# Kernel tuning notes

Hardware: AMD Instinct MI355X
Metric: run time of the kernel (lower is better)

## Reference

```python
import jax, jax.numpy as jnp
import numpy as np

N_NODES = 50000
N_EDGES = 1600000
IN_DIM = 128
N_HEADS = 8
OUT_DIM = 16  # output_dim // n_heads = 128 // 8


def setup_inputs() -> dict:
    key = jax.random.key(0)
    ks = jax.random.split(key, 8)
    feature = jax.random.normal(ks[0], (N_NODES, IN_DIM), dtype=jnp.float32)
    edge_src = jax.random.randint(ks[1], (N_EDGES,), 0, N_NODES)
    edge_dst = jax.random.randint(ks[2], (N_EDGES,), 0, N_NODES)
    edge_weight = jax.random.uniform(ks[3], (N_EDGES,), dtype=jnp.float32)
    w_lin = jax.random.normal(ks[4], (IN_DIM, N_HEADS * OUT_DIM), dtype=jnp.float32) * 0.1
    att_l = jax.random.normal(ks[5], (N_HEADS, OUT_DIM), dtype=jnp.float32) * 0.1
    att_r = jax.random.normal(ks[6], (N_HEADS, OUT_DIM), dtype=jnp.float32) * 0.1
    w_res = jax.random.normal(ks[7], (IN_DIM, N_HEADS * OUT_DIM), dtype=jnp.float32) * 0.1
    return {"feature": feature, "edge_src": edge_src, "edge_dst": edge_dst,
            "edge_weight": edge_weight, "w_lin": w_lin, "att_l": att_l,
            "att_r": att_r, "w_res": w_res}


def reference(feature, edge_src, edge_dst, edge_weight, w_lin, att_l, att_r, w_res):
    N = feature.shape[0]
    H, C = att_l.shape
    # Linear projection -> [N, H, C]
    x = (feature @ w_lin).reshape(N, H, C)
    # Per-node attention logits [N, H]
    al = jnp.einsum('nhc,hc->nh', x, att_l)
    ar = jnp.einsum('nhc,hc->nh', x, att_r)
    # Per-edge logits: gather src/dst, weight, leaky-relu  [E, H]
    alpha = al[edge_src] + ar[edge_dst]
    alpha = edge_weight[:, None] * alpha
    alpha = jax.nn.leaky_relu(alpha, negative_slope=0.2)
    # Segment softmax over edges grouped by destination node
    m = jax.ops.segment_max(alpha, edge_dst, num_segments=N)  # [N, H]
    m = jnp.where(jnp.isfinite(m), m, 0.0)
    e = jnp.exp(alpha - m[edge_dst])
    denom = jax.ops.segment_sum(e, edge_dst, num_segments=N)  # [N, H]
    coef = e / denom[edge_dst]                                 # [E, H]
    # Message passing: gather src feats, weight by coef, scatter-sum to dst
    msg = x[edge_src] * coef[:, :, None]                       # [E, H, C]
    feat = jax.ops.segment_sum(msg, edge_dst, num_segments=N)  # [N, H, C]
    out = jax.nn.elu(feat).reshape(N, H * C)
    out = out + feature @ w_res  # residual branch
    return out
```

## Files before the change

kernel.cpp:

```cpp
#include <hip/hip_runtime.h>
#include <math.h>

#define IN_DIM 128
#define NH 8
#define OC 16
#define HC 128
#define BSTR 136
#define ECH 4096
#define BINSZ 128
#define NBINS_MAX 512
#define FSTR 132
#define ALS 32

typedef __attribute__((ext_vector_type(8))) short short8;
typedef __attribute__((ext_vector_type(4))) float f32x4;

__device__ __forceinline__ unsigned short bf16_rne(float f) {
  unsigned int u = __builtin_bit_cast(unsigned int, f);
  u += 0x7FFFu + ((u >> 16) & 1u);
  return (unsigned short)(u >> 16);
}
__device__ __forceinline__ float bf16_to_f(unsigned short h) {
  unsigned int u = ((unsigned int)h) << 16;
  return __builtin_bit_cast(float, u);
}

__global__ __launch_bounds__(256) void k1_fused(const float* __restrict__ feature,
                                                const float* __restrict__ w_lin,
                                                const float* __restrict__ w_res,
                                                const float* __restrict__ att_l,
                                                const float* __restrict__ att_r,
                                                unsigned char* __restrict__ x8,
                                                unsigned char* __restrict__ als,
                                                float* __restrict__ ar,
                                                float* __restrict__ out,
                                                int* __restrict__ bin_cursor, int N) {
  __shared__ unsigned short BL[HC * BSTR];
  __shared__ unsigned short BR[HC * BSTR];
  __shared__ unsigned short WH[16 * BSTR];
  __shared__ unsigned short WL[16 * BSTR];
  const int t = threadIdx.x;
  if (blockIdx.x == 0) {
    bin_cursor[t] = 0;
    bin_cursor[t + 256] = 0;
  }
  for (int i = t; i < IN_DIM * HC; i += 256) {
    const int r = i >> 7, c = i & 127;
    BL[c * BSTR + r] = bf16_rne(w_lin[i]);
    BR[c * BSTR + r] = bf16_rne(w_res[i]);
  }
#pragma unroll
  for (int j = 0; j < 8; ++j) {
    const int idx = t * 8 + j;
    const int k = idx >> 4, c = idx & 15;
    const int h8 = c & 7;
    const float* __restrict__ av = ((c < 8) ? att_l : att_r) + h8 * OC;
    const float* __restrict__ wr = w_lin + k * HC + h8 * OC;
    float acc = 0.f;
#pragma unroll
    for (int oc = 0; oc < 16; ++oc) acc = fmaf(wr[oc], av[oc], acc);
    const unsigned short hi = bf16_rne(acc);
    WH[c * BSTR + k] = hi;
    WL[c * BSTR + k] = bf16_rne(acc - bf16_to_f(hi));
  }
  __syncthreads();

  const int wave = t >> 6, lane = t & 63;
  const int n16 = lane & 15, quad = lane >> 4;
  const int nStrips = (N + 15) >> 4;

  for (int strip = blockIdx.x * 4 + wave; strip < nStrips; strip += gridDim.x * 4) {
    const int row0 = strip * 16;
    const int arow = row0 + n16;
    const float* __restrict__ ap =
        feature + (size_t)((arow < N) ? arow : 0) * IN_DIM + quad * 8;
    short8 ahi[4], alo[4];
#pragma unroll
    for (int ks = 0; ks < 4; ++ks) {
      const float4 f0 = *(const float4*)(ap + ks * 32);
      const float4 f1 = *(const float4*)(ap + ks * 32 + 4);
      const float fv[8] = {f0.x, f0.y, f0.z, f0.w, f1.x, f1.y, f1.z, f1.w};
      short8 h, l;
#pragma unroll
      for (int j = 0; j < 8; ++j) {
        const unsigned short hh = bf16_rne(fv[j]);
        h[j] = (short)hh;
        l[j] = (short)bf16_rne(fv[j] - bf16_to_f(hh));
      }
      ahi[ks] = h;
      alo[ks] = l;
    }
    f32x4 xacc[8];
#pragma unroll
    for (int u = 0; u < 8; ++u) xacc[u] = (f32x4){0.f, 0.f, 0.f, 0.f};
#pragma unroll
    for (int ks = 0; ks < 4; ++ks) {
#pragma unroll
      for (int u = 0; u < 8; ++u) {
        const int boff = (u * 16 + n16) * BSTR + ks * 32 + quad * 8;
        const short8 bh = *(const short8*)&BL[boff];
        xacc[u] = __builtin_amdgcn_mfma_f32_16x16x32_bf16(ahi[ks], bh, xacc[u], 0, 0, 0);
        xacc[u] = __builtin_amdgcn_mfma_f32_16x16x32_bf16(alo[ks], bh, xacc[u], 0, 0, 0);
      }
    }
    {
      f32x4 accA = {0.f, 0.f, 0.f, 0.f};
#pragma unroll
      for (int ks = 0; ks < 4; ++ks) {
        const int boff = n16 * BSTR + ks * 32 + quad * 8;
        const short8 wh = *(const short8*)&WH[boff];
        const short8 wl = *(const short8*)&WL[boff];
        accA = __builtin_amdgcn_mfma_f32_16x16x32_bf16(ahi[ks], wh, accA, 0, 0, 0);
        accA = __builtin_amdgcn_mfma_f32_16x16x32_bf16(alo[ks], wh, accA, 0, 0, 0);
        accA = __builtin_amdgcn_mfma_f32_16x16x32_bf16(ahi[ks], wl, accA, 0, 0, 0);
      }
#pragma unroll
      for (int r = 0; r < 4; ++r) {
        const int rr = row0 + quad * 4 + r;
        if (rr < N) {
          if (n16 < 8) {
            *(unsigned short*)(als + (size_t)rr * ALS + n16 * 2) = bf16_rne(accA[r]);
          } else {
            ar[(size_t)rr * NH + (n16 - 8)] = accA[r];
          }
        }
      }
    }
    float m[4];
#pragma unroll
    for (int r = 0; r < 4; ++r) {
      float mm = 0.f;
#pragma unroll
      for (int u = 0; u < 8; ++u) mm = fmaxf(mm, fabsf(xacc[u][r]));
      mm = fmaxf(mm, __shfl_xor(mm, 1));
      mm = fmaxf(mm, __shfl_xor(mm, 2));
      mm = fmaxf(mm, __shfl_xor(mm, 4));
      mm = fmaxf(mm, __shfl_xor(mm, 8));
      m[r] = mm;
    }
#pragma unroll
    for (int r = 0; r < 4; ++r) {
      const int rr = row0 + quad * 4 + r;
      if (rr < N) {
        const float inv = (m[r] > 0.f) ? 127.f / m[r] : 0.f;
#pragma unroll
        for (int u = 0; u < 8; ++u) {
          const int q8 = (int)rintf(xacc[u][r] * inv) + 128;
          x8[(size_t)rr * HC + u * 16 + n16] = (unsigned char)q8;
        }
        if (n16 == 0)
          *(float*)(als + (size_t)rr * ALS + 16) = (m[r] > 0.f) ? m[r] / 127.f : 0.f;
      }
    }
#pragma unroll
    for (int cg = 0; cg < 2; ++cg) {
      f32x4 acc[4] = {{0.f,0.f,0.f,0.f},{0.f,0.f,0.f,0.f},{0.f,0.f,0.f,0.f},{0.f,0.f,0.f,0.f}};
#pragma unroll
      for (int ks = 0; ks < 4; ++ks) {
#pragma unroll
        for (int j = 0; j < 4; ++j) {
          const int boff = ((cg * 4 + j) * 16 + n16) * BSTR + ks * 32 + quad * 8;
          const short8 bh = *(const short8*)&BR[boff];
          acc[j] = __builtin_amdgcn_mfma_f32_16x16x32_bf16(ahi[ks], bh, acc[j], 0, 0, 0);
          acc[j] = __builtin_amdgcn_mfma_f32_16x16x32_bf16(alo[ks], bh, acc[j], 0, 0, 0);
        }
      }
#pragma unroll
      for (int j = 0; j < 4; ++j) {
        const int colo = (cg * 4 + j) * 16 + n16;
#pragma unroll
        for (int r = 0; r < 4; ++r) {
          const int rr = row0 + quad * 4 + r;
          if (rr < N) out[(size_t)rr * HC + colo] = acc[j][r];
        }
      }
    }
  }
}

__global__ __launch_bounds__(1024) void kb1_scatter(const int* __restrict__ esrc,
                                                    const int* __restrict__ edst,
                                                    const float* __restrict__ ew,
                                                    int* __restrict__ bin_cursor,
                                                    uint2* __restrict__ tmp,
                                                    int E, int nbins, int cap) {
  __shared__ int cnt[NBINS_MAX];
  __shared__ int gbase[NBINS_MAX];
  const int t = threadIdx.x;
  if (t < NBINS_MAX) cnt[t] = 0;
  __syncthreads();
  const int base = blockIdx.x * ECH;
  uint2 v[4];
  int bj[4], sj[4];
#pragma unroll
  for (int j = 0; j < 4; ++j) {
    const int e = base + j * 1024 + t;
    bj[j] = -1;
    if (e < E) {
      const int d = edst[e];
      v[j] = make_uint2((unsigned)esrc[e] | ((unsigned)(d & (BINSZ - 1)) << 16),
                        __float_as_uint(ew[e]));
      bj[j] = d >> 7;
      sj[j] = atomicAdd(&cnt[bj[j]], 1);
    }
  }
  __syncthreads();
  for (int b = t; b < nbins; b += 1024) {
    const int own = cnt[b];
    if (own > 0) gbase[b] = atomicAdd(&bin_cursor[b], own);
  }
  __syncthreads();
#pragma unroll
  for (int j = 0; j < 4; ++j)
    if (bj[j] >= 0) {
      const int p = gbase[bj[j]] + sj[j];
      if (p >= 0 && p < cap) tmp[(size_t)bj[j] * cap + p] = v[j];
    }
}

__global__ __launch_bounds__(1024) void kb3_sort(const uint2* __restrict__ tmp,
                                                 const int* __restrict__ bin_cursor,
                                                 uint2* __restrict__ packed,
                                                 int* __restrict__ row_start,
                                                 int cap, int nbins, int N) {
  const int b = blockIdx.x, t = threadIdx.x;
  const int M = bin_cursor[b];
  __shared__ int redw[16];
  int part = 0;
  for (int i = t; i < b; i += 1024) part += bin_cursor[i];
#pragma unroll
  for (int o = 32; o >= 1; o >>= 1) part += __shfl_xor(part, o);
  if ((t & 63) == 0) redw[t >> 6] = part;
  __syncthreads();
  int gstart = 0;
#pragma unroll
  for (int w = 0; w < 16; ++w) gstart += redw[w];
  if (b == nbins - 1 && t == 0) row_start[N] = gstart + M;

  const uint2* __restrict__ src = tmp + (size_t)b * cap;
  __shared__ int cnt[BINSZ];
  __shared__ int cur[BINSZ];
  __shared__ int s[BINSZ];
  if (t < BINSZ) cnt[t] = 0;
  __syncthreads();
  for (int i = t; i < M; i += 1024) atomicAdd(&cnt[src[i].x >> 16], 1);
  __syncthreads();
  if (t < BINSZ) s[t] = cnt[t];
  __syncthreads();
  for (int o = 1; o < BINSZ; o <<= 1) {
    int a = 0;
    if (t < BINSZ && t >= o) a = s[t - o];
    __syncthreads();
    if (t < BINSZ) s[t] += a;
    __syncthreads();
  }
  if (t < BINSZ) {
    const int ex = s[t] - cnt[t];
    cur[t] = gstart + ex;
    const int node = b * BINSZ + t;
    if (node < N) row_start[node] = gstart + ex;
  }
  __syncthreads();
  for (int i = t; i < M; i += 1024) {
    const uint2 v = src[i];
    const int pos = atomicAdd(&cur[v.x >> 16], 1);
    packed[pos] = make_uint2(v.x & 0xFFFFu, v.y);
  }
}

__global__ __launch_bounds__(64) void k5_agg(const unsigned char* __restrict__ x8,
                                             const unsigned char* __restrict__ als,
                                             const uint2* __restrict__ packed,
                                             const int* __restrict__ row_start,
                                             const float* __restrict__ ar,
                                             float* __restrict__ out, int N) {
  const int n = blockIdx.x;
  const int l = threadIdx.x;
  const int s0 = row_start[n];
  const int En = row_start[n + 1] - s0;
  if (En == 0) return;
  __shared__ int sbuf[64];
  __shared__ float wbuf[64];
  __shared__ float scbuf[64];
  __shared__ float fred[8 * FSTR];
  const int h = l & 7;
  const int g = l >> 3;
  const int ch0 = h * 16;

  const float arn = ar[(size_t)n * NH + h];
  float dpart = 0.f;
  float facsum = 0.f;
  float f[16];
#pragma unroll
  for (int j = 0; j < 16; ++j) f[j] = 0.f;

  for (int base = 0; base < En; base += 64) {
    const int cnt = min(64, En - base);
    __syncthreads();
    if (l < cnt) {
      const uint2 p = packed[s0 + base + l];
      const int src = (int)p.x;
      sbuf[l] = src;
      wbuf[l] = __uint_as_float(p.y);
      scbuf[l] = *(const float*)(als + (size_t)src * ALS + 16);
    }
    __syncthreads();
    for (int i = g; i < cnt; i += 8) {
      const int src = sbuf[i];
      const float aln =
          bf16_to_f(*(const unsigned short*)(als + (size_t)src * ALS + (h << 1)));
      float a = wbuf[i] * (aln + arn);
      a = (a > 0.f) ? a : 0.2f * a;
      const float e = __expf(a);
      dpart += e;
      const float fac = e * scbuf[i];
      facsum += fac;
      const int4 qw = *(const int4*)(x8 + (size_t)src * HC + ch0);
      const unsigned ux = (unsigned)qw.x, uy = (unsigned)qw.y;
      const unsigned uz = (unsigned)qw.z, uw = (unsigned)qw.w;
      f[0]  = fmaf(fac, (float)(ux & 0xFFu),         f[0]);
      f[1]  = fmaf(fac, (float)((ux >> 8) & 0xFFu),  f[1]);
      f[2]  = fmaf(fac, (float)((ux >> 16) & 0xFFu), f[2]);
      f[3]  = fmaf(fac, (float)(ux >> 24),           f[3]);
      f[4]  = fmaf(fac, (float)(uy & 0xFFu),         f[4]);
      f[5]  = fmaf(fac, (float)((uy >> 8) & 0xFFu),  f[5]);
      f[6]  = fmaf(fac, (float)((uy >> 16) & 0xFFu), f[6]);
      f[7]  = fmaf(fac, (float)(uy >> 24),           f[7]);
      f[8]  = fmaf(fac, (float)(uz & 0xFFu),         f[8]);
      f[9]  = fmaf(fac, (float)((uz >> 8) & 0xFFu),  f[9]);
      f[10] = fmaf(fac, (float)((uz >> 16) & 0xFFu), f[10]);
      f[11] = fmaf(fac, (float)(uz >> 24),           f[11]);
      f[12] = fmaf(fac, (float)(uw & 0xFFu),         f[12]);
      f[13] = fmaf(fac, (float)((uw >> 8) & 0xFFu),  f[13]);
      f[14] = fmaf(fac, (float)((uw >> 16) & 0xFFu), f[14]);
      f[15] = fmaf(fac, (float)(uw >> 24),           f[15]);
    }
  }
  dpart += __shfl_xor(dpart, 8);
  dpart += __shfl_xor(dpart, 16);
  dpart += __shfl_xor(dpart, 32);
  facsum += __shfl_xor(facsum, 8);
  facsum += __shfl_xor(facsum, 16);
  facsum += __shfl_xor(facsum, 32);
#pragma unroll
  for (int q = 0; q < 4; ++q) {
    const f32x4 v = {f[q * 4 + 0], f[q * 4 + 1], f[q * 4 + 2], f[q * 4 + 3]};
    *(f32x4*)&fred[g * FSTR + ch0 + q * 4] = v;
  }
  __syncthreads();
  float a0 = 0.f, a1 = 0.f;
#pragma unroll
  for (int gg = 0; gg < 8; ++gg) {
    const float2 v = *(const float2*)&fred[gg * FSTR + 2 * l];
    a0 += v.x;
    a1 += v.y;
  }
  const float dH = __shfl(dpart, l >> 3);
  const float fsH = __shfl(facsum, l >> 3);
  const float inv = 1.f / dH;
  float f0 = (a0 - 128.f * fsH) * inv;
  float f1 = (a1 - 128.f * fsH) * inv;
  f0 = (f0 > 0.f) ? f0 : (__expf(f0) - 1.f);
  f1 = (f1 > 0.f) ? f1 : (__expf(f1) - 1.f);
  float2 o = *(float2*)&out[(size_t)n * HC + 2 * l];
  o.x += f0;
  o.y += f1;
  *(float2*)&out[(size_t)n * HC + 2 * l] = o;
}

extern "C" void kernel_launch(void* const* d_in, const int* in_sizes, int n_in,
                              void* d_out, int out_size, void* d_ws, size_t ws_size,
                              hipStream_t stream) {
  const float* feature = (const float*)d_in[0];
  const int* esrc = (const int*)d_in[1];
  const int* edst = (const int*)d_in[2];
  const float* ew = (const float*)d_in[3];
  const float* w_lin = (const float*)d_in[4];
  const float* att_l = (const float*)d_in[5];
  const float* att_r = (const float*)d_in[6];
  const float* w_res = (const float*)d_in[7];
  float* out = (float*)d_out;

  const int N = in_sizes[0] / IN_DIM;
  const int E = in_sizes[1];
  const int nbins = (N + BINSZ - 1) / BINSZ;
  int cap = (E + nbins - 1) / nbins;
  cap = cap + cap / 4 + 512;
  cap = (cap + 63) & ~63;
  const int nch = (E + ECH - 1) / ECH;

  char* ws = (char*)d_ws;
  size_t off = 0;
  auto alloc = [&](size_t bytes) {
    void* p = ws + off;
    off = (off + bytes + 255) & ~(size_t)255;
    return p;
  };
  uint2* tmp = (uint2*)alloc((size_t)nbins * cap * sizeof(uint2));
  unsigned char* x8 = (unsigned char*)alloc((size_t)N * HC);
  unsigned char* als = (unsigned char*)alloc((size_t)N * ALS);
  float* ar = (float*)alloc((size_t)N * NH * sizeof(float));
  int* row_start = (int*)alloc((size_t)(N + 1) * sizeof(int));
  int* bin_cursor = (int*)alloc((size_t)NBINS_MAX * sizeof(int));
  uint2* packed = (uint2*)alloc((size_t)E * sizeof(uint2));

  k1_fused<<<512, 256, 0, stream>>>(feature, w_lin, w_res, att_l, att_r,
                                    x8, als, ar, out, bin_cursor, N);
  kb1_scatter<<<nch, 1024, 0, stream>>>(esrc, edst, ew, bin_cursor, tmp, E, nbins, cap);
  kb3_sort<<<nbins, 1024, 0, stream>>>(tmp, bin_cursor, packed, row_start, cap, nbins, N);
  k5_agg<<<N, 64, 0, stream>>>(x8, als, packed, row_start, ar, out, N);
}
```

Before: 192.3 us.

## Replace two-pass bin sort with global atomic count, scan, and scatter CSR build

Replaces the bucketed two-level CSR construction (scatter edges into 128-node bins, then per-bin LDS counting sort) with a classic three-kernel approach: per-node global atomic histogram, block-wise prefix scan, and atomic-cursor scatter directly into the packed edge array. This removes the intermediate tmp buffer pass and its extra read/write of all edges. In exchange it issues two global atomics per edge with random addresses, and the scan kernel recomputes prefix sums by re-reading row counts quadratically across blocks. Edge order within a row becomes nondeterministic.

```diff
diff --git a/kernel.cpp b/kernel.cpp
--- a/kernel.cpp
+++ b/kernel.cpp
@@ -6,9 +6,6 @@
 #define OC 16
 #define HC 128
 #define BSTR 136
-#define ECH 4096
-#define BINSZ 128
-#define NBINS_MAX 512
 #define FSTR 132
 #define ALS 32
 
@@ -34,15 +31,17 @@
                                                 unsigned char* __restrict__ als,
                                                 float* __restrict__ ar,
                                                 float* __restrict__ out,
-                                                int* __restrict__ bin_cursor, int N) {
+                                                int* __restrict__ row_count, int N) {
   __shared__ unsigned short BL[HC * BSTR];
   __shared__ unsigned short BR[HC * BSTR];
   __shared__ unsigned short WH[16 * BSTR];
   __shared__ unsigned short WL[16 * BSTR];
   const int t = threadIdx.x;
-  if (blockIdx.x == 0) {
-    bin_cursor[t] = 0;
-    bin_cursor[t + 256] = 0;
+  {
+    const int zc = (N + gridDim.x - 1) / gridDim.x;
+    const int z0 = blockIdx.x * zc;
+    const int z1 = min(z0 + zc, N);
+    for (int i = z0 + t; i < z1; i += 256) row_count[i] = 0;
   }
   for (int i = t; i < IN_DIM * HC; i += 256) {
     const int r = i >> 7, c = i & 127;
@@ -178,93 +177,83 @@
   }
 }
 
-__global__ __launch_bounds__(1024) void kb1_scatter(const int* __restrict__ esrc,
-                                                    const int* __restrict__ edst,
-                                                    const float* __restrict__ ew,
-                                                    int* __restrict__ bin_cursor,
-                                                    uint2* __restrict__ tmp,
-                                                    int E, int nbins, int cap) {
-  __shared__ int cnt[NBINS_MAX];
-  __shared__ int gbase[NBINS_MAX];
-  const int t = threadIdx.x;
-  if (t < NBINS_MAX) cnt[t] = 0;
-  __syncthreads();
-  const int base = blockIdx.x * ECH;
-  uint2 v[4];
-  int bj[4], sj[4];
-#pragma unroll
-  for (int j = 0; j < 4; ++j) {
-    const int e = base + j * 1024 + t;
-    bj[j] = -1;
-    if (e < E) {
-      const int d = edst[e];
-      v[j] = make_uint2((unsigned)esrc[e] | ((unsigned)(d & (BINSZ - 1)) << 16),
-                        __float_as_uint(ew[e]));
-      bj[j] = d >> 7;
-      sj[j] = atomicAdd(&cnt[bj[j]], 1);
-    }
-  }
-  __syncthreads();
-  for (int b = t; b < nbins; b += 1024) {
-    const int own = cnt[b];
-    if (own > 0) gbase[b] = atomicAdd(&bin_cursor[b], own);
-  }
-  __syncthreads();
-#pragma unroll
-  for (int j = 0; j < 4; ++j)
-    if (bj[j] >= 0) {
-      const int p = gbase[bj[j]] + sj[j];
-      if (p >= 0 && p < cap) tmp[(size_t)bj[j] * cap + p] = v[j];
-    }
-}
-
-__global__ __launch_bounds__(1024) void kb3_sort(const uint2* __restrict__ tmp,
-                                                 const int* __restrict__ bin_cursor,
-                                                 uint2* __restrict__ packed,
-                                                 int* __restrict__ row_start,
-                                                 int cap, int nbins, int N) {
+__global__ __launch_bounds__(256) void ka_count(const int* __restrict__ edst,
+                                                int* __restrict__ row_count, int E) {
+  const int e0 = (blockIdx.x * 256 + threadIdx.x) * 8;
+#pragma unroll
+  for (int j = 0; j < 8; j += 4) {
+    const int e = e0 + j;
+    if (e + 3 < E) {
+      const int4 d4 = *(const int4*)(edst + e);
+      atomicAdd(&row_count[d4.x], 1);
+      atomicAdd(&row_count[d4.y], 1);
+      atomicAdd(&row_count[d4.z], 1);
+      atomicAdd(&row_count[d4.w], 1);
+    } else {
+      for (int k = e; k < E; ++k)
+        if (k < e + 4) atomicAdd(&row_count[edst[k]], 1);
+    }
+  }
+}
+
+__global__ __launch_bounds__(256) void kb_scan(const int* __restrict__ row_count,
+                                               int* __restrict__ row_start,
+                                               int* __restrict__ cursor,
+                                               int nb, int N) {
   const int b = blockIdx.x, t = threadIdx.x;
-  const int M = bin_cursor[b];
-  __shared__ int redw[16];
   int part = 0;
-  for (int i = t; i < b; i += 1024) part += bin_cursor[i];
+  for (int i = t; i < b * 256; i += 256) part += row_count[i];
 #pragma unroll
   for (int o = 32; o >= 1; o >>= 1) part += __shfl_xor(part, o);
+  __shared__ int redw[4];
   if ((t & 63) == 0) redw[t >> 6] = part;
   __syncthreads();
-  int gstart = 0;
-#pragma unroll
-  for (int w = 0; w < 16; ++w) gstart += redw[w];
-  if (b == nbins - 1 && t == 0) row_start[N] = gstart + M;
-
-  const uint2* __restrict__ src = tmp + (size_t)b * cap;
-  __shared__ int cnt[BINSZ];
-  __shared__ int cur[BINSZ];
-  __shared__ int s[BINSZ];
-  if (t < BINSZ) cnt[t] = 0;
+  const int gstart = redw[0] + redw[1] + redw[2] + redw[3];
+
+  __shared__ int s[256];
+  const int node = b * 256 + t;
+  const int own = (node < N) ? row_count[node] : 0;
+  s[t] = own;
   __syncthreads();
-  for (int i = t; i < M; i += 1024) atomicAdd(&cnt[src[i].x >> 16], 1);
-  __syncthreads();
-  if (t < BINSZ) s[t] = cnt[t];
-  __syncthreads();
-  for (int o = 1; o < BINSZ; o <<= 1) {
-    int a = 0;
-    if (t < BINSZ && t >= o) a = s[t - o];
+  for (int o = 1; o < 256; o <<= 1) {
+    const int a = (t >= o) ? s[t - o] : 0;
     __syncthreads();
-    if (t < BINSZ) s[t] += a;
+    s[t] += a;
     __syncthreads();
   }
-  if (t < BINSZ) {
-    const int ex = s[t] - cnt[t];
-    cur[t] = gstart + ex;
-    const int node = b * BINSZ + t;
-    if (node < N) row_start[node] = gstart + ex;
-  }
-  __syncthreads();
-  for (int i = t; i < M; i += 1024) {
-    const uint2 v = src[i];
-    const int pos = atomicAdd(&cur[v.x >> 16], 1);
-    packed[pos] = make_uint2(v.x & 0xFFFFu, v.y);
+  if (node < N) {
+    const int ex = gstart + s[t] - own;
+    row_start[node] = ex;
+    cursor[node] = ex;
+  }
+  if (b == nb - 1 && t == 255) row_start[N] = gstart + s[255];
+}
+
+__global__ __launch_bounds__(256) void kc_scatter(const int* __restrict__ esrc,
+                                                  const int* __restrict__ edst,
+                                                  const float* __restrict__ ew,
+                                                  int* __restrict__ cursor,
+                                                  uint2* __restrict__ packed, int E) {
+  const int e0 = (blockIdx.x * 256 + threadIdx.x) * 4;
+  if (e0 + 3 < E) {
+    const int4 s4 = *(const int4*)(esrc + e0);
+    const int4 d4 = *(const int4*)(edst + e0);
+    const float4 w4 = *(const float4*)(ew + e0);
+    int p;
+    p = atomicAdd(&cursor[d4.x], 1);
+    packed[p] = make_uint2((unsigned)s4.x, __float_as_uint(w4.x));
+    p = atomicAdd(&cursor[d4.y], 1);
+    packed[p] = make_uint2((unsigned)s4.y, __float_as_uint(w4.y));
+    p = atomicAdd(&cursor[d4.z], 1);
+    packed[p] = make_uint2((unsigned)s4.z, __float_as_uint(w4.z));
+    p = atomicAdd(&cursor[d4.w], 1);
+    packed[p] = make_uint2((unsigned)s4.w, __float_as_uint(w4.w));
+  } else {
+    for (int e = e0; e < E; ++e) {
+      if (e >= e0 + 4) break;
+      const int p = atomicAdd(&cursor[edst[e]], 1);
+      packed[p] = make_uint2((unsigned)esrc[e], __float_as_uint(ew[e]));
+    }
   }
 }
 
@@ -383,11 +372,6 @@
 
   const int N = in_sizes[0] / IN_DIM;
   const int E = in_sizes[1];
-  const int nbins = (N + BINSZ - 1) / BINSZ;
-  int cap = (E + nbins - 1) / nbins;
-  cap = cap + cap / 4 + 512;
-  cap = (cap + 63) & ~63;
-  const int nch = (E + ECH - 1) / ECH;
 
   char* ws = (char*)d_ws;
   size_t off = 0;
@@ -396,17 +380,22 @@
     off = (off + bytes + 255) & ~(size_t)255;
     return p;
   };
-  uint2* tmp = (uint2*)alloc((size_t)nbins * cap * sizeof(uint2));
   unsigned char* x8 = (unsigned char*)alloc((size_t)N * HC);
   unsigned char* als = (unsigned char*)alloc((size_t)N * ALS);
   float* ar = (float*)alloc((size_t)N * NH * sizeof(float));
+  int* row_count = (int*)alloc((size_t)N * sizeof(int));
   int* row_start = (int*)alloc((size_t)(N + 1) * sizeof(int));
-  int* bin_cursor = (int*)alloc((size_t)NBINS_MAX * sizeof(int));
+  int* cursor = (int*)alloc((size_t)N * sizeof(int));
   uint2* packed = (uint2*)alloc((size_t)E * sizeof(uint2));
 
+  const int nbA = (E + 2047) / 2048;
+  const int nbB = (N + 255) / 256;
+  const int nbC = (E + 1023) / 1024;
+
   k1_fused<<<512, 256, 0, stream>>>(feature, w_lin, w_res, att_l, att_r,
-                                    x8, als, ar, out, bin_cursor, N);
-  kb1_scatter<<<nch, 1024, 0, stream>>>(esrc, edst, ew, bin_cursor, tmp, E, nbins, cap);
-  kb3_sort<<<nbins, 1024, 0, stream>>>(tmp, bin_cursor, packed, row_start, cap, nbins, N);
+                                    x8, als, ar, out, row_count, N);
+  ka_count<<<nbA, 256, 0, stream>>>(edst, row_count, E);
+  kb_scan<<<nbB, 256, 0, stream>>>(row_count, row_start, cursor, nbB, N);
+  kc_scatter<<<nbC, 256, 0, stream>>>(esrc, edst, ew, cursor, packed, E);
   k5_agg<<<N, 64, 0, stream>>>(x8, als, packed, row_start, ar, out, N);
 }
```

Result: slower. 366.1 us (+90.3%).

## Count per-node degrees in bin scatter and split CSR sort into scan plus scatter

Applied to the files above, without the earlier changes.

Per-destination edge counts are now accumulated with global atomics during the binning pass, and a separate scan kernel builds row_start and per-node cursors. The per-bin sort kernel is replaced by a simple scatter that uses global atomics on those cursors, which removes the in-block histogram and shared-memory scan. In exchange it adds one kernel launch and 1.6M global atomics in the binning pass. The scan kernel also re-reads row_count prefixes on every block, which is quadratic in the number of blocks.

```diff
diff --git a/kernel.cpp b/kernel.cpp
--- a/kernel.cpp
+++ b/kernel.cpp
@@ -34,6 +34,7 @@
                                                 unsigned char* __restrict__ als,
                                                 float* __restrict__ ar,
                                                 float* __restrict__ out,
+                                                int* __restrict__ row_count,
                                                 int* __restrict__ bin_cursor, int N) {
   __shared__ unsigned short BL[HC * BSTR];
   __shared__ unsigned short BR[HC * BSTR];
@@ -44,6 +45,12 @@
     bin_cursor[t] = 0;
     bin_cursor[t + 256] = 0;
   }
+  {
+    const int zc = (N + gridDim.x - 1) / gridDim.x;
+    const int z0 = blockIdx.x * zc;
+    const int z1 = min(z0 + zc, N);
+    for (int i = z0 + t; i < z1; i += 256) row_count[i] = 0;
+  }
   for (int i = t; i < IN_DIM * HC; i += 256) {
     const int r = i >> 7, c = i & 127;
     BL[c * BSTR + r] = bf16_rne(w_lin[i]);
@@ -182,6 +189,7 @@
                                                     const int* __restrict__ edst,
                                                     const float* __restrict__ ew,
                                                     int* __restrict__ bin_cursor,
+                                                    int* __restrict__ row_count,
                                                     uint2* __restrict__ tmp,
                                                     int E, int nbins, int cap) {
   __shared__ int cnt[NBINS_MAX];
@@ -202,6 +210,7 @@
                         __float_as_uint(ew[e]));
       bj[j] = d >> 7;
       sj[j] = atomicAdd(&cnt[bj[j]], 1);
+      atomicAdd(&row_count[d], 1);
     }
   }
   __syncthreads();
@@ -218,52 +227,52 @@
     }
 }
 
-__global__ __launch_bounds__(1024) void kb3_sort(const uint2* __restrict__ tmp,
-                                                 const int* __restrict__ bin_cursor,
-                                                 uint2* __restrict__ packed,
-                                                 int* __restrict__ row_start,
-                                                 int cap, int nbins, int N) {
+__global__ __launch_bounds__(256) void kb_scan(const int* __restrict__ row_count,
+                                               int* __restrict__ row_start,
+                                               int* __restrict__ cursor,
+                                               int nb, int N) {
   const int b = blockIdx.x, t = threadIdx.x;
+  int part = 0;
+  for (int i = t; i < b * 256; i += 256) part += row_count[i];
+#pragma unroll
+  for (int o = 32; o >= 1; o >>= 1) part += __shfl_xor(part, o);
+  __shared__ int redw[4];
+  if ((t & 63) == 0) redw[t >> 6] = part;
+  __syncthreads();
+  const int gstart = redw[0] + redw[1] + redw[2] + redw[3];
+
+  __shared__ int s[256];
+  const int node = b * 256 + t;
+  const int own = (node < N) ? row_count[node] : 0;
+  s[t] = own;
+  __syncthreads();
+  for (int o = 1; o < 256; o <<= 1) {
+    const int a = (t >= o) ? s[t - o] : 0;
+    __syncthreads();
+    s[t] += a;
+    __syncthreads();
+  }
+  if (node < N) {
+    const int ex = gstart + s[t] - own;
+    row_start[node] = ex;
+    cursor[node] = ex;
+  }
+  if (b == nb - 1 && t == 255) row_start[N] = gstart + s[255];
+}
+
+__global__ __launch_bounds__(1024) void kb3_scatter(const uint2* __restrict__ tmp,
+                                                    const int* __restrict__ bin_cursor,
+                                                    int* __restrict__ cursor,
+                                                    uint2* __restrict__ packed,
+                                                    int cap) {
+  const int b = blockIdx.x;
   const int M = bin_cursor[b];
-  __shared__ int redw[16];
-  int part = 0;
-  for (int i = t; i < b; i += 1024) part += bin_cursor[i];
-#pragma unroll
-  for (int o = 32; o >= 1; o >>= 1) part += __shfl_xor(part, o);
-  if ((t & 63) == 0) redw[t >> 6] = part;
-  __syncthreads();
-  int gstart = 0;
-#pragma unroll
-  for (int w = 0; w < 16; ++w) gstart += redw[w];
-  if (b == nbins - 1 && t == 0) row_start[N] = gstart + M;
-
   const uint2* __restrict__ src = tmp + (size_t)b * cap;
-  __shared__ int cnt[BINSZ];
-  __shared__ int cur[BINSZ];
-  __shared__ int s[BINSZ];
-  if (t < BINSZ) cnt[t] = 0;
-  __syncthreads();
-  for (int i = t; i < M; i += 1024) atomicAdd(&cnt[src[i].x >> 16], 1);
-  __syncthreads();
-  if (t < BINSZ) s[t] = cnt[t];
-  __syncthreads();
-  for (int o = 1; o < BINSZ; o <<= 1) {
-    int a = 0;
-    if (t < BINSZ && t >= o) a = s[t - o];
-    __syncthreads();
-    if (t < BINSZ) s[t] += a;
-    __syncthreads();
-  }
-  if (t < BINSZ) {
-    const int ex = s[t] - cnt[t];
-    cur[t] = gstart + ex;
-    const int node = b * BINSZ + t;
-    if (node < N) row_start[node] = gstart + ex;
-  }
-  __syncthreads();
-  for (int i = t; i < M; i += 1024) {
+  const int binbase = b * BINSZ;
+  for (int i = threadIdx.x; i < M; i += 1024) {
     const uint2 v = src[i];
-    const int pos = atomicAdd(&cur[v.x >> 16], 1);
+    const int d = binbase + (int)(v.x >> 16);
+    const int pos = atomicAdd(&cursor[d], 1);
     packed[pos] = make_uint2(v.x & 0xFFFFu, v.y);
   }
 }
@@ -388,6 +397,7 @@
   cap = cap + cap / 4 + 512;
   cap = (cap + 63) & ~63;
   const int nch = (E + ECH - 1) / ECH;
+  const int nbB = (N + 255) / 256;
 
   char* ws = (char*)d_ws;
   size_t off = 0;
@@ -400,13 +410,17 @@
   unsigned char* x8 = (unsigned char*)alloc((size_t)N * HC);
   unsigned char* als = (unsigned char*)alloc((size_t)N * ALS);
   float* ar = (float*)alloc((size_t)N * NH * sizeof(float));
+  int* row_count = (int*)alloc((size_t)N * sizeof(int));
   int* row_start = (int*)alloc((size_t)(N + 1) * sizeof(int));
+  int* cursor = (int*)alloc((size_t)N * sizeof(int));
   int* bin_cursor = (int*)alloc((size_t)NBINS_MAX * sizeof(int));
   uint2* packed = (uint2*)alloc((size_t)E * sizeof(uint2));
 
   k1_fused<<<512, 256, 0, stream>>>(feature, w_lin, w_res, att_l, att_r,
-                                    x8, als, ar, out, bin_cursor, N);
-  kb1_scatter<<<nch, 1024, 0, stream>>>(esrc, edst, ew, bin_cursor, tmp, E, nbins, cap);
-  kb3_sort<<<nbins, 1024, 0, stream>>>(tmp, bin_cursor, packed, row_start, cap, nbins, N);
+                                    x8, als, ar, out, row_count, bin_cursor, N);
+  kb1_scatter<<<nch, 1024, 0, stream>>>(esrc, edst, ew, bin_cursor, row_count,
+                                        tmp, E, nbins, cap);
+  kb_scan<<<nbB, 256, 0, stream>>>(row_count, row_start, cursor, nbB, N);
+  kb3_scatter<<<nbins, 1024, 0, stream>>>(tmp, bin_cursor, cursor, packed, cap);
   k5_agg<<<N, 64, 0, stream>>>(x8, als, packed, row_start, ar, out, N);
 }
```

Result: slower. 310.9 us (+61.7%).
